# Performance work log

Measured on AMD Instinct MI355X. Metric: run time of the kernel, lower is better.

## Reference

```python
import jax, jax.numpy as jnp
import numpy as np

EPSILON = 1e-06
N_TOKENS = 65536
WIDTH_IN = 1024
WIDTH_OUT = 1024
NUM_HEAD = 16
DIM_HEAD = 64


def setup_inputs() -> dict:
    key = jax.random.key(0)
    k_x, k_b, k_lin, k_ker = jax.random.split(key, 4)
    x = jax.random.normal(k_x, (N_TOKENS, WIDTH_IN), dtype=jnp.float32)
    norm_bias = jax.random.normal(k_b, (N_TOKENS, NUM_HEAD, DIM_HEAD), dtype=jnp.float32)
    # LinearLayer: std = 1/sqrt(width_in), shape (width_in, num_head*dim_head)
    w_lin = jax.random.normal(k_lin, (WIDTH_IN, NUM_HEAD * DIM_HEAD), dtype=jnp.float32) / np.sqrt(WIDTH_IN)
    # Grouped kernel: (num_head, dim_head, width_out // num_head), scaled 1/sqrt(dim_head)
    kernel = jax.random.normal(k_ker, (NUM_HEAD, DIM_HEAD, WIDTH_OUT // NUM_HEAD), dtype=jnp.float32) / np.sqrt(DIM_HEAD)
    return {"x": x, "norm_bias": norm_bias, "w_lin": w_lin, "kernel": kernel}


def reference(x, norm_bias, w_lin, kernel):
    # Dense projection, bias-free
    xx = x @ w_lin                                   # [N, H*D]
    xx = xx.reshape(*x.shape[:-1], NUM_HEAD, DIM_HEAD)  # [N, H, D]
    # Per-head RMSNorm
    xx = xx / jnp.sqrt(jnp.mean(jnp.square(xx), axis=-1, keepdims=True) + EPSILON)
    # Optional norm-bias blend
    xx = (xx + norm_bias.reshape(xx.shape)) / 2 ** 0.5
    # Per-head grouped matmul
    xx = jnp.einsum('nhd,hdf->nhf', xx, kernel)      # [N, H, F]
    return xx.reshape(*x.shape[:-1], -1)             # [N, H*F]
```

## Files before the change

### kernel.cpp

```cpp
#include <hip/hip_runtime.h>


typedef __attribute__((ext_vector_type(8))) __bf16 bf16x8;
typedef __attribute__((ext_vector_type(4))) float f32x4;
typedef __attribute__((ext_vector_type(8))) unsigned short ushort8;

__device__ __forceinline__ unsigned short bfbits(float f) {
  return __builtin_bit_cast(unsigned short, (__bf16)f);
}
__device__ __forceinline__ f32x4 mfma_bf16(bf16x8 a, bf16x8 b, f32x4 c) {
  return __builtin_amdgcn_mfma_f32_16x16x32_bf16(a, b, c, 0, 0, 0);
}
__device__ __forceinline__ void gl_lds16(const void* g, void* l) {
  __builtin_amdgcn_global_load_lds(
      (const __attribute__((address_space(1))) unsigned int*)g,
      (__attribute__((address_space(3))) unsigned int*)l, 16, 0, 0);
}

__global__ void cvt_x(const float* __restrict__ x, unsigned short* __restrict__ xb, int n8) {
  int i = blockIdx.x * blockDim.x + threadIdx.x;
  const int stride = gridDim.x * blockDim.x;
  for (; i < n8; i += stride) {
    f32x4 a = *reinterpret_cast<const f32x4*>(x + (size_t)i * 8);
    f32x4 b = *reinterpret_cast<const f32x4*>(x + (size_t)i * 8 + 4);
    ushort8 v;
    v[0] = bfbits(a[0]); v[1] = bfbits(a[1]); v[2] = bfbits(a[2]); v[3] = bfbits(a[3]);
    v[4] = bfbits(b[0]); v[5] = bfbits(b[1]); v[6] = bfbits(b[2]); v[7] = bfbits(b[3]);
    *reinterpret_cast<ushort8*>(xb + (size_t)i * 8) = v;
  }
}

__global__ void prep_w(const float* __restrict__ w, unsigned short* __restrict__ wb) {
  const int img = blockIdx.x;
  const int ct = img >> 5, ktg = (img >> 1) & 15, half = img & 1;
  #pragma unroll
  for (int i = 0; i < 4; ++i) {
    const int q = i * 256 + threadIdx.x;
    const int c = q >> 3, s = q & 7;
    const int k0 = ktg * 64 + 8 * (s ^ (c & 7));
    const int col = ct * 256 + half * 128 + c;
    ushort8 v;
    #pragma unroll
    for (int j = 0; j < 8; ++j) v[j] = bfbits(w[(size_t)(k0 + j) * 1024 + col]);
    *reinterpret_cast<ushort8*>(wb + (size_t)img * 8192 + (size_t)q * 8) = v;
  }
}

__global__ void transpose_k(const float* __restrict__ kin, unsigned short* __restrict__ kt) {
  __shared__ float tile[64][65];
  const int h = blockIdx.x;
  const int t = threadIdx.x;
  #pragma unroll
  for (int i = 0; i < 16; ++i) {
    int idx = i * 256 + t;
    tile[idx >> 6][idx & 63] = kin[(size_t)h * 4096 + idx];
  }
  __syncthreads();
  #pragma unroll
  for (int i = 0; i < 16; ++i) {
    int idx = i * 256 + t;
    kt[(size_t)h * 4096 + idx] = bfbits(tile[idx & 63][idx >> 6]);
  }
}

__global__ __launch_bounds__(512, 2)
void fused_main(const unsigned short* __restrict__ xb,
                const float* __restrict__ nbias,
                const unsigned short* __restrict__ wb,
                const unsigned short* __restrict__ ktg_,
                float* __restrict__ out)
{
  __shared__ __align__(16) unsigned char smem[131072];
  const int tid = threadIdx.x;
  const int wv = tid >> 6, lane = tid & 63, l15 = lane & 15, lg = lane >> 4;
  const int l7 = l15 & 7;
  const int wr = wv >> 2, wc = wv & 3;
  const int bid = blockIdx.x;
  const int v = (bid & 7) * 128 + (bid >> 3);
  const int rt = v >> 2, ct = v & 3;
  const size_t row0 = (size_t)rt * 256;

  const char* xB = (const char*)xb;
  const char* wB = (const char*)wb + (size_t)ct * 524288;

  const int su = tid >> 3, ss = tid & 7;
  const char* asrc = xB + (row0 + su) * 2048 + ((ss ^ (su & 7)) << 4);

  const int aO0 = wr * 16384 + l15 * 128 + ((lg ^ l7) << 4);
  const int aO1 = wr * 16384 + l15 * 128 + (((4 + lg) ^ l7) << 4);
  const int bH  = 65536 + (wc >> 1) * 16384 + ((wc & 1) * 64 + l15) * 128;
  const int bO0 = bH + ((lg ^ l7) << 4);
  const int bO1 = bH + (((4 + lg) ^ l7) << 4);

  f32x4 acc[8][4];
  const f32x4 z4 = {0.f, 0.f, 0.f, 0.f};
  #pragma unroll
  for (int mi = 0; mi < 8; ++mi)
    #pragma unroll
    for (int ni = 0; ni < 4; ++ni) acc[mi][ni] = z4;

  auto stageA2 = [&](int kt, int buf) {
    unsigned char* d = smem + (buf << 15) + tid * 16;
    const char* s0 = asrc + (size_t)kt * 128;
    gl_lds16(s0,          d);
    gl_lds16(s0 + 131072, d + 8192);
    gl_lds16(s0 + 262144, d + 16384);
    gl_lds16(s0 + 393216, d + 24576);
  };
  auto stageB2 = [&](int kt, int buf) {
    unsigned char* d = smem + 65536 + (buf << 15) + tid * 16;
    const char* s0 = wB + (size_t)kt * 32768 + tid * 16;
    gl_lds16(s0,         d);
    gl_lds16(s0 + 8192,  d + 8192);
    gl_lds16(s0 + 16384, d + 16384);
    gl_lds16(s0 + 24576, d + 24576);
  };

  stageA2(0, 0);
  stageB2(0, 0);
  asm volatile("s_waitcnt vmcnt(0)" ::: "memory");
  __builtin_amdgcn_s_barrier();

  for (int tau = 0; tau < 16; ++tau) {
    const int cb = tau & 1, nb = cb ^ 1;
    const bool st = (tau + 1 < 16);
    const unsigned char* S = smem + (cb << 15);
    bf16x8 alo[4][2], ahi[4][2], blo[2][2], bhi[2][2];

    #pragma unroll
    for (int m = 0; m < 4; ++m) {
      alo[m][0] = *reinterpret_cast<const bf16x8*>(S + aO0 + m * 2048);
      alo[m][1] = *reinterpret_cast<const bf16x8*>(S + aO1 + m * 2048);
    }
    #pragma unroll
    for (int n = 0; n < 2; ++n) {
      blo[n][0] = *reinterpret_cast<const bf16x8*>(S + bO0 + n * 2048);
      blo[n][1] = *reinterpret_cast<const bf16x8*>(S + bO1 + n * 2048);
    }
    if (st) stageA2(tau + 1, nb);
    __builtin_amdgcn_s_barrier();
    asm volatile("s_waitcnt lgkmcnt(0)" ::: "memory");
    __builtin_amdgcn_s_setprio(1);
    #pragma unroll
    for (int m = 0; m < 4; ++m)
      #pragma unroll
      for (int n = 0; n < 2; ++n)
        acc[m][n] = mfma_bf16(alo[m][1], blo[n][1],
                    mfma_bf16(alo[m][0], blo[n][0], acc[m][n]));
    __builtin_amdgcn_s_setprio(0);
    __builtin_amdgcn_s_barrier();

    #pragma unroll
    for (int n = 0; n < 2; ++n) {
      bhi[n][0] = *reinterpret_cast<const bf16x8*>(S + bO0 + (2 + n) * 2048);
      bhi[n][1] = *reinterpret_cast<const bf16x8*>(S + bO1 + (2 + n) * 2048);
    }
    if (st) stageB2(tau + 1, nb);
    __builtin_amdgcn_s_barrier();
    asm volatile("s_waitcnt lgkmcnt(0)" ::: "memory");
    __builtin_amdgcn_s_setprio(1);
    #pragma unroll
    for (int m = 0; m < 4; ++m)
      #pragma unroll
      for (int n = 0; n < 2; ++n)
        acc[m][2 + n] = mfma_bf16(alo[m][1], bhi[n][1],
                        mfma_bf16(alo[m][0], bhi[n][0], acc[m][2 + n]));
    __builtin_amdgcn_s_setprio(0);
    __builtin_amdgcn_s_barrier();

    #pragma unroll
    for (int m = 0; m < 4; ++m) {
      ahi[m][0] = *reinterpret_cast<const bf16x8*>(S + aO0 + (4 + m) * 2048);
      ahi[m][1] = *reinterpret_cast<const bf16x8*>(S + aO1 + (4 + m) * 2048);
    }
    __builtin_amdgcn_s_barrier();
    asm volatile("s_waitcnt lgkmcnt(0)" ::: "memory");
    __builtin_amdgcn_s_setprio(1);
    #pragma unroll
    for (int m = 0; m < 4; ++m)
      #pragma unroll
      for (int n = 0; n < 2; ++n)
        acc[4 + m][n] = mfma_bf16(ahi[m][1], blo[n][1],
                        mfma_bf16(ahi[m][0], blo[n][0], acc[4 + m][n]));
    __builtin_amdgcn_s_setprio(0);
    __builtin_amdgcn_s_barrier();

    __builtin_amdgcn_s_setprio(1);
    #pragma unroll
    for (int m = 0; m < 4; ++m)
      #pragma unroll
      for (int n = 0; n < 2; ++n)
        acc[4 + m][2 + n] = mfma_bf16(ahi[m][1], bhi[n][1],
                            mfma_bf16(ahi[m][0], bhi[n][0], acc[4 + m][2 + n]));
    __builtin_amdgcn_s_setprio(0);
    if (st) asm volatile("s_waitcnt vmcnt(0)" ::: "memory");
    __builtin_amdgcn_s_barrier();
  }
  __syncthreads();

  const int h = ct * 4 + wc;
  unsigned short* yw = reinterpret_cast<unsigned short*>(smem + wv * 16384);
  const float* bb = nbias + (row0 + wr * 128) * 1024 + (size_t)h * 64 + l15;

  #pragma unroll
  for (int mi = 0; mi < 8; ++mi) {
    float ssq[4];
    #pragma unroll
    for (int r = 0; r < 4; ++r) {
      float p = 0.f;
      #pragma unroll
      for (int ni = 0; ni < 4; ++ni) { const float q = acc[mi][ni][r]; p += q * q; }
      ssq[r] = p;
    }
    #pragma unroll
    for (int s = 1; s < 16; s <<= 1)
      #pragma unroll
      for (int r = 0; r < 4; ++r) ssq[r] += __shfl_xor(ssq[r], s, 64);
    #pragma unroll
    for (int r = 0; r < 4; ++r) {
      const float rs = rsqrtf(ssq[r] * 0.015625f + 1e-6f);
      const int rl = mi * 16 + lg * 4 + r;
      const float* bp = bb + (size_t)rl * 1024;
      #pragma unroll
      for (int ni = 0; ni < 4; ++ni) {
        const float y = (acc[mi][ni][r] * rs + bp[ni * 16]) * 0.70710678118654752f;
        const int sy = (ni * 2 + (l15 >> 3)) ^ (rl & 7);
        yw[rl * 64 + sy * 8 + l7] = bfbits(y);
      }
    }
  }
  asm volatile("s_waitcnt lgkmcnt(0)" ::: "memory");

  const unsigned short* ktp = ktg_ + (size_t)h * 4096;
  bf16x8 b2[4][2];
  #pragma unroll
  for (int ff = 0; ff < 4; ++ff)
    #pragma unroll
    for (int ks = 0; ks < 2; ++ks)
      b2[ff][ks] = *reinterpret_cast<const bf16x8*>(ktp + (ff * 16 + l15) * 64 + ks * 32 + lg * 8);

  #pragma unroll
  for (int m2 = 0; m2 < 8; ++m2) {
    f32x4 a2[4] = {z4, z4, z4, z4};
    const int row = m2 * 16 + l15;
    #pragma unroll
    for (int ks = 0; ks < 2; ++ks) {
      const int sl = ((ks * 4 + lg) ^ l7);
      bf16x8 a = *reinterpret_cast<const bf16x8*>(yw + row * 64 + sl * 8);
      #pragma unroll
      for (int ff = 0; ff < 4; ++ff) a2[ff] = mfma_bf16(a, b2[ff][ks], a2[ff]);
    }
    float* ob = out + (row0 + wr * 128 + m2 * 16 + lg * 4) * 1024 + h * 64 + l15;
    #pragma unroll
    for (int ff = 0; ff < 4; ++ff)
      #pragma unroll
      for (int r = 0; r < 4; ++r)
        ob[(size_t)r * 1024 + ff * 16] = a2[ff][r];
  }
}

extern "C" void kernel_launch(void* const* d_in, const int* in_sizes, int n_in,
                              void* d_out, int out_size, void* d_ws, size_t ws_size,
                              hipStream_t stream) {
  const float* x  = (const float*)d_in[0];
  const float* nb = (const float*)d_in[1];
  const float* wl = (const float*)d_in[2];
  const float* kr = (const float*)d_in[3];
  float* out = (float*)d_out;

  unsigned short* wbp = (unsigned short*)d_ws;
  unsigned short* ktp = wbp + 1048576;
  unsigned short* xbp = (unsigned short*)((char*)d_ws + 2228224);

  hipLaunchKernelGGL(prep_w, dim3(128), dim3(256), 0, stream, wl, wbp);
  hipLaunchKernelGGL(transpose_k, dim3(16), dim3(256), 0, stream, kr, ktp);
  hipLaunchKernelGGL(cvt_x, dim3(2048), dim3(256), 0, stream, x, xbp, 65536 * 128);
  hipLaunchKernelGGL(fused_main, dim3(1024), dim3(512), 0, stream, xbp, nb, wbp, ktp, out);
}
```

Before: 305.8 us.

## Pre-tile X and W into LDS images and use 4-stage K=32 pipeline

The conversion kernels now write X and W as per-tile contiguous bf16 images in an MFMA-fragment order, so LDS fragment reads become simple strided loads with no XOR swizzle. The main GEMM loop drops from two buffers of K=64 to four buffers of K=32 with three tiles in flight, waiting on partial vmcnt counts instead of draining all loads each step. This aims to hide global-load latency better and to simplify address math. The unswizzled LDS layout may add bank conflicts, and each step does less MFMA work relative to its barriers.

```diff
diff --git a/kernel.cpp b/kernel.cpp
--- a/kernel.cpp
+++ b/kernel.cpp
@@ -17,33 +17,29 @@
       (__attribute__((address_space(3))) unsigned int*)l, 16, 0, 0);
 }
 
-__global__ void cvt_x(const float* __restrict__ x, unsigned short* __restrict__ xb, int n8) {
-  int i = blockIdx.x * blockDim.x + threadIdx.x;
-  const int stride = gridDim.x * blockDim.x;
-  for (; i < n8; i += stride) {
-    f32x4 a = *reinterpret_cast<const f32x4*>(x + (size_t)i * 8);
-    f32x4 b = *reinterpret_cast<const f32x4*>(x + (size_t)i * 8 + 4);
+__global__ void cvt_x_img(const float* __restrict__ x, unsigned short* __restrict__ img) {
+  const int rt = blockIdx.x, t = blockIdx.y, u = threadIdx.x;
+  const float* src = x + ((size_t)rt * 256 + u) * 1024 + t * 32;
+  unsigned short* dst = img + ((size_t)rt * 32 + t) * 8192;
+  #pragma unroll
+  for (int j = 0; j < 4; ++j) {
+    f32x4 a = *reinterpret_cast<const f32x4*>(src + j * 8);
+    f32x4 b = *reinterpret_cast<const f32x4*>(src + j * 8 + 4);
     ushort8 v;
     v[0] = bfbits(a[0]); v[1] = bfbits(a[1]); v[2] = bfbits(a[2]); v[3] = bfbits(a[3]);
     v[4] = bfbits(b[0]); v[5] = bfbits(b[1]); v[6] = bfbits(b[2]); v[7] = bfbits(b[3]);
-    *reinterpret_cast<ushort8*>(xb + (size_t)i * 8) = v;
+    *reinterpret_cast<ushort8*>(dst + (size_t)(j * 256 + u) * 8) = v;
   }
 }
 
 __global__ void prep_w(const float* __restrict__ w, unsigned short* __restrict__ wb) {
-  const int img = blockIdx.x;
-  const int ct = img >> 5, ktg = (img >> 1) & 15, half = img & 1;
-  #pragma unroll
-  for (int i = 0; i < 4; ++i) {
-    const int q = i * 256 + threadIdx.x;
-    const int c = q >> 3, s = q & 7;
-    const int k0 = ktg * 64 + 8 * (s ^ (c & 7));
-    const int col = ct * 256 + half * 128 + c;
-    ushort8 v;
-    #pragma unroll
-    for (int j = 0; j < 8; ++j) v[j] = bfbits(w[(size_t)(k0 + j) * 1024 + col]);
-    *reinterpret_cast<ushort8*>(wb + (size_t)img * 8192 + (size_t)q * 8) = v;
-  }
+  const int g = blockIdx.x * 256 + threadIdx.x;
+  const int col = g & 255, kc = (g >> 8) & 3, t = (g >> 10) & 31, ct = g >> 15;
+  const int k0 = t * 32 + kc * 8;
+  ushort8 v;
+  #pragma unroll
+  for (int j = 0; j < 8; ++j) v[j] = bfbits(w[(size_t)(k0 + j) * 1024 + ct * 256 + col]);
+  *reinterpret_cast<ushort8*>(wb + (size_t)g * 8) = v;
 }
 
 __global__ void transpose_k(const float* __restrict__ kin, unsigned short* __restrict__ kt) {
@@ -64,7 +60,7 @@
 }
 
 __global__ __launch_bounds__(512, 2)
-void fused_main(const unsigned short* __restrict__ xb,
+void fused_main(const unsigned short* __restrict__ ximg,
                 const float* __restrict__ nbias,
                 const unsigned short* __restrict__ wb,
                 const unsigned short* __restrict__ ktg_,
@@ -80,17 +76,11 @@
   const int rt = v >> 2, ct = v & 3;
   const size_t row0 = (size_t)rt * 256;
 
-  const char* xB = (const char*)xb;
-  const char* wB = (const char*)wb + (size_t)ct * 524288;
-
-  const int su = tid >> 3, ss = tid & 7;
-  const char* asrc = xB + (row0 + su) * 2048 + ((ss ^ (su & 7)) << 4);
-
-  const int aO0 = wr * 16384 + l15 * 128 + ((lg ^ l7) << 4);
-  const int aO1 = wr * 16384 + l15 * 128 + (((4 + lg) ^ l7) << 4);
-  const int bH  = 65536 + (wc >> 1) * 16384 + ((wc & 1) * 64 + l15) * 128;
-  const int bO0 = bH + ((lg ^ l7) << 4);
-  const int bO1 = bH + (((4 + lg) ^ l7) << 4);
+  const char* aimg = (const char*)ximg + (size_t)rt * 524288 + tid * 16;
+  const char* bimg = (const char*)wb + (size_t)ct * 524288 + tid * 16;
+
+  const int aBase = lg * 4096 + (wr * 128 + l15) * 16;
+  const int bBase = lg * 4096 + (wc * 64 + l15) * 16;
 
   f32x4 acc[8][4];
   const f32x4 z4 = {0.f, 0.f, 0.f, 0.f};
@@ -99,103 +89,75 @@
     #pragma unroll
     for (int ni = 0; ni < 4; ++ni) acc[mi][ni] = z4;
 
-  auto stageA2 = [&](int kt, int buf) {
-    unsigned char* d = smem + (buf << 15) + tid * 16;
-    const char* s0 = asrc + (size_t)kt * 128;
-    gl_lds16(s0,          d);
-    gl_lds16(s0 + 131072, d + 8192);
-    gl_lds16(s0 + 262144, d + 16384);
-    gl_lds16(s0 + 393216, d + 24576);
+  auto stageA = [&](int t, int bsel) {
+    unsigned char* d = smem + (bsel << 14) + tid * 16;
+    const char* s = aimg + (size_t)t * 16384;
+    gl_lds16(s, d);
+    gl_lds16(s + 8192, d + 8192);
   };
-  auto stageB2 = [&](int kt, int buf) {
-    unsigned char* d = smem + 65536 + (buf << 15) + tid * 16;
-    const char* s0 = wB + (size_t)kt * 32768 + tid * 16;
-    gl_lds16(s0,         d);
-    gl_lds16(s0 + 8192,  d + 8192);
-    gl_lds16(s0 + 16384, d + 16384);
-    gl_lds16(s0 + 24576, d + 24576);
+  auto stageB = [&](int t, int bsel) {
+    unsigned char* d = smem + 65536 + (bsel << 14) + tid * 16;
+    const char* s = bimg + (size_t)t * 16384;
+    gl_lds16(s, d);
+    gl_lds16(s + 8192, d + 8192);
   };
 
-  stageA2(0, 0);
-  stageB2(0, 0);
+  auto tile_compute = [&](int csel, int ssel, bool doStage, int stageT) {
+    const unsigned char* Ab = smem + (csel << 14);
+    const unsigned char* Bb = smem + 65536 + (csel << 14);
+    bf16x8 afr[4], bfr[4], ahr[4];
+    #pragma unroll
+    for (int m = 0; m < 4; ++m)
+      afr[m] = *reinterpret_cast<const bf16x8*>(Ab + aBase + m * 256);
+    #pragma unroll
+    for (int n = 0; n < 4; ++n)
+      bfr[n] = *reinterpret_cast<const bf16x8*>(Bb + bBase + n * 256);
+    if (doStage) stageA(stageT, ssel);
+    __builtin_amdgcn_s_barrier();
+    asm volatile("s_waitcnt lgkmcnt(0)" ::: "memory");
+    __builtin_amdgcn_sched_barrier(0);
+    __builtin_amdgcn_s_setprio(1);
+    #pragma unroll
+    for (int m = 0; m < 4; ++m)
+      #pragma unroll
+      for (int n = 0; n < 4; ++n)
+        acc[m][n] = mfma_bf16(afr[m], bfr[n], acc[m][n]);
+    __builtin_amdgcn_s_setprio(0);
+    __builtin_amdgcn_s_barrier();
+    #pragma unroll
+    for (int m = 0; m < 4; ++m)
+      ahr[m] = *reinterpret_cast<const bf16x8*>(Ab + aBase + (4 + m) * 256);
+    if (doStage) stageB(stageT, ssel);
+    __builtin_amdgcn_s_barrier();
+    asm volatile("s_waitcnt lgkmcnt(0)" ::: "memory");
+    __builtin_amdgcn_sched_barrier(0);
+    __builtin_amdgcn_s_setprio(1);
+    #pragma unroll
+    for (int m = 0; m < 4; ++m)
+      #pragma unroll
+      for (int n = 0; n < 4; ++n)
+        acc[4 + m][n] = mfma_bf16(ahr[m], bfr[n], acc[4 + m][n]);
+    __builtin_amdgcn_s_setprio(0);
+  };
+
+  stageA(0, 0); stageB(0, 0);
+  stageA(1, 1); stageB(1, 1);
+  stageA(2, 2); stageB(2, 2);
+  asm volatile("s_waitcnt vmcnt(8)" ::: "memory");
+  __builtin_amdgcn_s_barrier();
+
+  for (int t = 0; t < 29; ++t) {
+    tile_compute(t & 3, (t + 3) & 3, true, t + 3);
+    asm volatile("s_waitcnt vmcnt(8)" ::: "memory");
+    __builtin_amdgcn_s_barrier();
+  }
+  tile_compute(1, 0, false, 0);
+  asm volatile("s_waitcnt vmcnt(4)" ::: "memory");
+  __builtin_amdgcn_s_barrier();
+  tile_compute(2, 0, false, 0);
   asm volatile("s_waitcnt vmcnt(0)" ::: "memory");
   __builtin_amdgcn_s_barrier();
-
-  for (int tau = 0; tau < 16; ++tau) {
-    const int cb = tau & 1, nb = cb ^ 1;
-    const bool st = (tau + 1 < 16);
-    const unsigned char* S = smem + (cb << 15);
-    bf16x8 alo[4][2], ahi[4][2], blo[2][2], bhi[2][2];
-
-    #pragma unroll
-    for (int m = 0; m < 4; ++m) {
-      alo[m][0] = *reinterpret_cast<const bf16x8*>(S + aO0 + m * 2048);
-      alo[m][1] = *reinterpret_cast<const bf16x8*>(S + aO1 + m * 2048);
-    }
-    #pragma unroll
-    for (int n = 0; n < 2; ++n) {
-      blo[n][0] = *reinterpret_cast<const bf16x8*>(S + bO0 + n * 2048);
-      blo[n][1] = *reinterpret_cast<const bf16x8*>(S + bO1 + n * 2048);
-    }
-    if (st) stageA2(tau + 1, nb);
-    __builtin_amdgcn_s_barrier();
-    asm volatile("s_waitcnt lgkmcnt(0)" ::: "memory");
-    __builtin_amdgcn_s_setprio(1);
-    #pragma unroll
-    for (int m = 0; m < 4; ++m)
-      #pragma unroll
-      for (int n = 0; n < 2; ++n)
-        acc[m][n] = mfma_bf16(alo[m][1], blo[n][1],
-                    mfma_bf16(alo[m][0], blo[n][0], acc[m][n]));
-    __builtin_amdgcn_s_setprio(0);
-    __builtin_amdgcn_s_barrier();
-
-    #pragma unroll
-    for (int n = 0; n < 2; ++n) {
-      bhi[n][0] = *reinterpret_cast<const bf16x8*>(S + bO0 + (2 + n) * 2048);
-      bhi[n][1] = *reinterpret_cast<const bf16x8*>(S + bO1 + (2 + n) * 2048);
-    }
-    if (st) stageB2(tau + 1, nb);
-    __builtin_amdgcn_s_barrier();
-    asm volatile("s_waitcnt lgkmcnt(0)" ::: "memory");
-    __builtin_amdgcn_s_setprio(1);
-    #pragma unroll
-    for (int m = 0; m < 4; ++m)
-      #pragma unroll
-      for (int n = 0; n < 2; ++n)
-        acc[m][2 + n] = mfma_bf16(alo[m][1], bhi[n][1],
-                        mfma_bf16(alo[m][0], bhi[n][0], acc[m][2 + n]));
-    __builtin_amdgcn_s_setprio(0);
-    __builtin_amdgcn_s_barrier();
-
-    #pragma unroll
-    for (int m = 0; m < 4; ++m) {
-      ahi[m][0] = *reinterpret_cast<const bf16x8*>(S + aO0 + (4 + m) * 2048);
-      ahi[m][1] = *reinterpret_cast<const bf16x8*>(S + aO1 + (4 + m) * 2048);
-    }
-    __builtin_amdgcn_s_barrier();
-    asm volatile("s_waitcnt lgkmcnt(0)" ::: "memory");
-    __builtin_amdgcn_s_setprio(1);
-    #pragma unroll
-    for (int m = 0; m < 4; ++m)
-      #pragma unroll
-      for (int n = 0; n < 2; ++n)
-        acc[4 + m][n] = mfma_bf16(ahi[m][1], blo[n][1],
-                        mfma_bf16(ahi[m][0], blo[n][0], acc[4 + m][n]));
-    __builtin_amdgcn_s_setprio(0);
-    __builtin_amdgcn_s_barrier();
-
-    __builtin_amdgcn_s_setprio(1);
-    #pragma unroll
-    for (int m = 0; m < 4; ++m)
-      #pragma unroll
-      for (int n = 0; n < 2; ++n)
-        acc[4 + m][2 + n] = mfma_bf16(ahi[m][1], bhi[n][1],
-                            mfma_bf16(ahi[m][0], bhi[n][0], acc[4 + m][2 + n]));
-    __builtin_amdgcn_s_setprio(0);
-    if (st) asm volatile("s_waitcnt vmcnt(0)" ::: "memory");
-    __builtin_amdgcn_s_barrier();
-  }
+  tile_compute(3, 0, false, 0);
   __syncthreads();
 
   const int h = ct * 4 + wc;
@@ -270,10 +232,10 @@
 
   unsigned short* wbp = (unsigned short*)d_ws;
   unsigned short* ktp = wbp + 1048576;
-  unsigned short* xbp = (unsigned short*)((char*)d_ws + 2228224);
-
-  hipLaunchKernelGGL(prep_w, dim3(128), dim3(256), 0, stream, wl, wbp);
+  unsigned short* xip = (unsigned short*)((char*)d_ws + 2228224);
+
+  hipLaunchKernelGGL(prep_w, dim3(512), dim3(256), 0, stream, wl, wbp);
   hipLaunchKernelGGL(transpose_k, dim3(16), dim3(256), 0, stream, kr, ktp);
-  hipLaunchKernelGGL(cvt_x, dim3(2048), dim3(256), 0, stream, x, xbp, 65536 * 128);
-  hipLaunchKernelGGL(fused_main, dim3(1024), dim3(512), 0, stream, xbp, nb, wbp, ktp, out);
-}
+  hipLaunchKernelGGL(cvt_x_img, dim3(256, 32), dim3(256), 0, stream, x, xip);
+  hipLaunchKernelGGL(fused_main, dim3(1024), dim3(512), 0, stream, xip, nb, wbp, ktp, out);
+}
```

Result: slower. 323.8 us (+5.9%).
